# Kernel tuning notes

Measured on AMD Instinct MI355X. Metric: run time of the kernel, lower is better.

The kernel has to match this reference:

```python
import jax, jax.numpy as jnp
import numpy as np

DECAY = 0.8
EPS = 1e-05


def setup_inputs() -> dict:
    key = jax.random.key(0)
    k_x, k_e = jax.random.split(key)
    x = jax.random.normal(k_x, (8, 4096, 256), dtype=jnp.float32)
    embed = jax.random.normal(k_e, (8192, 256), dtype=jnp.float32)
    cluster_size = jnp.zeros((8192,), dtype=jnp.float32)
    embed_avg = embed  # buffer initialized as embed.clone()
    return {"x": x, "embed": embed, "cluster_size": cluster_size, "embed_avg": embed_avg}


def reference(x, embed, cluster_size, embed_avg):
    shape = x.shape
    K, d = embed.shape
    flatten = x.reshape(-1, d)  # [N, d]

    dist = -(jnp.sum(flatten * flatten, axis=1, keepdims=True)
             - 2.0 * (flatten @ embed.T)
             + jnp.sum(embed * embed, axis=1)[None, :])  # [N, K]
    embed_ind = jnp.argmax(dist, axis=-1)  # [N]

    quantize = jnp.take(embed, embed_ind, axis=0).reshape(shape)
    embed_ind_out = embed_ind.reshape(shape[:-1])

    # Training-mode EMA update (one_hot sum / one_hot matmul expressed as scatter-adds)
    counts = jnp.zeros((K,), dtype=x.dtype).at[embed_ind].add(1.0)  # embed_onehot.sum(0)
    embed_sum = jnp.zeros((K, d), dtype=x.dtype).at[embed_ind].add(flatten)  # (flatten^T @ onehot)^T

    new_cluster_size = cluster_size * DECAY + counts * (1.0 - DECAY)
    new_embed_avg = embed_avg * DECAY + embed_sum * (1.0 - DECAY)

    smoothed = (new_cluster_size + EPS) / (new_cluster_size.sum() + K * EPS) * new_cluster_size.sum()
    new_embed = new_embed_avg / smoothed[:, None]

    return quantize, embed_ind_out, new_cluster_size, new_embed_avg, new_embed
```

## Files before the change

### kernel.cpp

```cpp
#include <hip/hip_runtime.h>

#define N_ROWS 32768
#define DIM    256
#define KCODES 8192
#define DECAYF 0.8f
#define OMDF   0.2f
#define EPSF   1e-5f

#define Q_OFF    0
#define IND_OFF  8388608
#define CS_OFF   8421376
#define EA_OFF   8429568
#define NE_OFF   10526720


#define WS_E2    0
#define WS_CNT   8192
#define WS_START 16384
#define WS_CUR   24576
#define WS_SUM   40960

typedef _Float16 half8 __attribute__((ext_vector_type(8)));
typedef float floatx16 __attribute__((ext_vector_type(16)));

#define GLOAD16(g, l) __builtin_amdgcn_global_load_lds( \
    (const __attribute__((address_space(1))) void*)(g), \
    (__attribute__((address_space(3))) void*)(l), 16, 0, 0)

__global__ void zero1_kernel(const float* __restrict__ cs,
                             float* __restrict__ out, float* __restrict__ ws) {
  __shared__ float red[4];
  const int t = threadIdx.x;
  int g = blockIdx.x * blockDim.x + t;
  unsigned long long* gbest = (unsigned long long*)(out + EA_OFF);
  gbest[g] = 0ULL;
  if (g < KCODES) ((int*)(ws + WS_CNT))[g] = 0;
  if (blockIdx.x == 0) {
    float s = 0.0f;
    for (int j = t; j < KCODES; j += 256) s += cs[j];
    #pragma unroll
    for (int o = 32; o; o >>= 1) s += __shfl_xor(s, o);
    if ((t & 63) == 0) red[t >> 6] = s;
    __syncthreads();
    if (t == 0) ws[WS_SUM] = red[0] + red[1] + red[2] + red[3];
  }
}

#define PREP_ROWS 32
__global__ void prep_x_kernel(const float* __restrict__ x,
                              _Float16* __restrict__ Xp) {
  __shared__ __align__(16) _Float16 L[PREP_ROWS][264];
  const int t = threadIdx.x;
  const int row0 = blockIdx.x * PREP_ROWS;
  #pragma unroll
  for (int it = 0; it < 8; ++it) {
    int idx = it * 256 + t;
    int r = idx >> 6, q = idx & 63;
    float4 v = *(const float4*)&x[(size_t)(row0 + r) * DIM + q * 4];
    L[r][q * 4 + 0] = (_Float16)v.x;
    L[r][q * 4 + 1] = (_Float16)v.y;
    L[r][q * 4 + 2] = (_Float16)v.z;
    L[r][q * 4 + 3] = (_Float16)v.w;
  }
  __syncthreads();
  #pragma unroll
  for (int it = 0; it < 4; ++it) {
    int idx = it * 256 + t;
    int slot = idx >> 5, r = idx & 31;
    *(float4*)&Xp[((size_t)slot * N_ROWS + row0 + r) * 8] =
        *(const float4*)&L[r][slot * 8];
  }
}

__global__ void prep_e_kernel(const float* __restrict__ embed,
                              _Float16* __restrict__ Ep,
                              float* __restrict__ e2) {
  __shared__ __align__(16) _Float16 L[PREP_ROWS][264];
  const int t = threadIdx.x;
  const int row0 = blockIdx.x * PREP_ROWS;
  #pragma unroll
  for (int it = 0; it < 8; ++it) {
    int idx = it * 256 + t;
    int r = idx >> 6, q = idx & 63;
    float4 v = *(const float4*)&embed[(size_t)(row0 + r) * DIM + q * 4];
    L[r][q * 4 + 0] = (_Float16)v.x;
    L[r][q * 4 + 1] = (_Float16)v.y;
    L[r][q * 4 + 2] = (_Float16)v.z;
    L[r][q * 4 + 3] = (_Float16)v.w;
    float ssq = v.x * v.x + v.y * v.y + v.z * v.z + v.w * v.w;
    #pragma unroll
    for (int o = 32; o; o >>= 1) ssq += __shfl_xor(ssq, o);
    if ((t & 63) == 0) e2[row0 + r] = ssq;
  }
  __syncthreads();
  #pragma unroll
  for (int it = 0; it < 4; ++it) {
    int idx = it * 256 + t;
    int slot = idx >> 5, r = idx & 31;
    *(float4*)&Ep[((size_t)slot * KCODES + row0 + r) * 8] =
        *(const float4*)&L[r][slot * 8];
  }
}

__global__ __launch_bounds__(512, 2) void main_kernel(
    const _Float16* __restrict__ Xp, const _Float16* __restrict__ Ep,
    const float* __restrict__ e2, unsigned long long* __restrict__ gbest) {
  __shared__ __align__(16) _Float16 As[4 * 4 * 256 * 8];
  __shared__ __align__(16) _Float16 Bs[4 * 4 * 256 * 8];
  __shared__ __align__(16) float e2s[256];

  const int t = threadIdx.x;
  const int w = t >> 6;
  const int lane = t & 63;
  const int l31 = lane & 31;
  const int h = lane >> 5;
  const int wm = w >> 2;
  const int wn = w & 3;

  const int bid = blockIdx.x;
  const int bi = bid >> 3;
  const int cb = (bid & 7) * 4 + (bi >> 5);
  const int rbg = bi & 31;
  const int codes0 = cb * 256;
  const int rowbase = rbg * 1024;

  const bool isA = (w < 4);
  const int slot = isA ? w : (w - 4);

  auto stage = [&](int s) {
    const int buf = s & 3;
    const int se = (s & 7) * 4 + slot;
    if (isA) {
      const _Float16* src = Ep + ((size_t)se * KCODES + codes0 + lane) * 8;
      _Float16* dst = &As[buf * 8192 + slot * 2048];
      #pragma unroll
      for (int q = 0; q < 4; ++q)
        GLOAD16(src + q * 512, dst + q * 512);
    } else {
      const int row0 = rowbase + (s >> 3) * 256;
      const _Float16* src = Xp + ((size_t)se * N_ROWS + row0 + lane) * 8;
      _Float16* dst = &Bs[buf * 8192 + slot * 2048];
      #pragma unroll
      for (int q = 0; q < 4; ++q)
        GLOAD16(src + q * 512, dst + q * 512);
    }
  };

  if (t < 64) {
    float4 v = *(const float4*)&e2[codes0 + t * 4];
    *(float4*)&e2s[t * 4] = v;
  }
  __builtin_amdgcn_sched_barrier(0);
  stage(0);
  stage(1);
  asm volatile("s_waitcnt vmcnt(4)" ::: "memory");
  asm volatile("s_waitcnt lgkmcnt(0)" ::: "memory");
  __builtin_amdgcn_s_barrier();
  __builtin_amdgcn_sched_barrier(0);

  floatx16 acc[4][2];
  unsigned long long pbest[4][2];

  #pragma unroll
  for (int tile = 0; tile < 4; ++tile) {
    #pragma unroll
    for (int ct = 0; ct < 4; ++ct) {
      const int cl = wm * 128 + ct * 32 + 4 * h;
      #pragma unroll
      for (int rq = 0; rq < 4; ++rq) {
        float4 v = *(const float4*)&e2s[cl + rq * 8];
        acc[ct][0][rq * 4 + 0] = -0.5f * v.x;
        acc[ct][0][rq * 4 + 1] = -0.5f * v.y;
        acc[ct][0][rq * 4 + 2] = -0.5f * v.z;
        acc[ct][0][rq * 4 + 3] = -0.5f * v.w;
      }
      acc[ct][1] = acc[ct][0];
    }

    #pragma unroll 1
    for (int i = 0; i < 8; ++i) {
      const int s = tile * 8 + i;
      if (s + 2 < 32) stage(s + 2);
      __builtin_amdgcn_sched_barrier(0);

      const int cur = (i & 3) * 8192;
      #pragma unroll
      for (int ks = 0; ks < 2; ++ks) {
        const int sbase = cur + (2 * ks + h) * 2048;
        half8 a0 = *(const half8*)&As[sbase + (wm * 128 + l31) * 8];
        half8 a1 = *(const half8*)&As[sbase + (wm * 128 + 32 + l31) * 8];
        half8 a2 = *(const half8*)&As[sbase + (wm * 128 + 64 + l31) * 8];
        half8 a3 = *(const half8*)&As[sbase + (wm * 128 + 96 + l31) * 8];
        half8 b0 = *(const half8*)&Bs[sbase + (wn * 64 + l31) * 8];
        half8 b1 = *(const half8*)&Bs[sbase + (wn * 64 + 32 + l31) * 8];
        __builtin_amdgcn_s_setprio(1);
        acc[0][0] = __builtin_amdgcn_mfma_f32_32x32x16_f16(a0, b0, acc[0][0], 0, 0, 0);
        acc[0][1] = __builtin_amdgcn_mfma_f32_32x32x16_f16(a0, b1, acc[0][1], 0, 0, 0);
        acc[1][0] = __builtin_amdgcn_mfma_f32_32x32x16_f16(a1, b0, acc[1][0], 0, 0, 0);
        acc[1][1] = __builtin_amdgcn_mfma_f32_32x32x16_f16(a1, b1, acc[1][1], 0, 0, 0);
        acc[2][0] = __builtin_amdgcn_mfma_f32_32x32x16_f16(a2, b0, acc[2][0], 0, 0, 0);
        acc[2][1] = __builtin_amdgcn_mfma_f32_32x32x16_f16(a2, b1, acc[2][1], 0, 0, 0);
        acc[3][0] = __builtin_amdgcn_mfma_f32_32x32x16_f16(a3, b0, acc[3][0], 0, 0, 0);
        acc[3][1] = __builtin_amdgcn_mfma_f32_32x32x16_f16(a3, b1, acc[3][1], 0, 0, 0);
        __builtin_amdgcn_s_setprio(0);
      }
      __builtin_amdgcn_sched_barrier(0);

      if (s < 31) {
        if (s < 30) {
          asm volatile("s_waitcnt vmcnt(4)" ::: "memory");
        } else {
          asm volatile("s_waitcnt vmcnt(0)" ::: "memory");
        }
        __builtin_amdgcn_s_barrier();
        __builtin_amdgcn_sched_barrier(0);
      }
    }

    #pragma unroll
    for (int rt = 0; rt < 2; ++rt) {
      float best = -3.0e38f;
      int bidx = 0;
      #pragma unroll
      for (int ct = 0; ct < 4; ++ct) {
        const int cbase = codes0 + wm * 128 + ct * 32 + 4 * h;
        #pragma unroll
        for (int r = 0; r < 16; ++r) {
          const int code = cbase + (r & 3) + 8 * (r >> 2);
          float v = acc[ct][rt][r];
          if (v > best || (v == best && code < bidx)) { best = v; bidx = code; }
        }
      }
      unsigned u = __float_as_uint(best);
      u = (u & 0x80000000u) ? ~u : (u | 0x80000000u);
      unsigned long long p =
          ((unsigned long long)u << 32) | (unsigned)(8191 - bidx);
      unsigned long long op = (unsigned long long)__shfl_xor((long long)p, 32);
      if (op > p) p = op;
      pbest[tile][rt] = p;
    }
  }

  #pragma unroll
  for (int tile = 0; tile < 4; ++tile)
    #pragma unroll
    for (int rt = 0; rt < 2; ++rt)
      if (h == 0)
        atomicMax(&gbest[rowbase + tile * 256 + wn * 64 + rt * 32 + l31],
                  pbest[tile][rt]);
}

__global__ void finish_q_kernel(const float* __restrict__ embed,
                                const unsigned long long* __restrict__ gbest,
                                float* __restrict__ out, int* __restrict__ cnt) {
  const int lane = threadIdx.x & 63;
  const int wave = (blockIdx.x * blockDim.x + threadIdx.x) >> 6;
  for (int row = wave; row < N_ROWS; row += 2048) {
    unsigned long long p = gbest[row];
    int k = 8191 - (int)(unsigned)(p & 0xFFFFFFFFull);
    float4 ev = *(const float4*)&embed[(size_t)k * DIM + lane * 4];
    *(float4*)&out[Q_OFF + (size_t)row * DIM + lane * 4] = ev;
    if (lane == 0) {
      out[IND_OFF + row] = (float)k;
      atomicAdd(&cnt[k], 1);
    }
  }
}

__global__ void prefix_kernel(const int* __restrict__ cnt,
                              int* __restrict__ start,
                              int* __restrict__ cursor) {
  __shared__ int part[1024];
  const int t = threadIdx.x;
  int loc[8];
  int s = 0;
  #pragma unroll
  for (int j = 0; j < 8; ++j) { loc[j] = cnt[t * 8 + j]; s += loc[j]; }
  part[t] = s;
  __syncthreads();
  for (int off = 1; off < 1024; off <<= 1) {
    int v = (t >= off) ? part[t - off] : 0;
    __syncthreads();
    part[t] += v;
    __syncthreads();
  }
  int base = part[t] - s;
  #pragma unroll
  for (int j = 0; j < 8; ++j) {
    start[t * 8 + j] = base;
    cursor[t * 8 + j] = base;
    base += loc[j];
  }
}

__global__ void scatter_rows_kernel(const float* __restrict__ out,
                                    int* __restrict__ cursor,
                                    int* __restrict__ rowlist) {
  int r = blockIdx.x * blockDim.x + threadIdx.x;
  int k = (int)out[IND_OFF + r];
  int pos = atomicAdd(&cursor[k], 1);
  rowlist[pos] = r;
}

__global__ void bucket_sum_kernel(const float* __restrict__ x,
                                  const float* __restrict__ cs,
                                  const int* __restrict__ start,
                                  const int* __restrict__ cnt,
                                  const int* __restrict__ rowlist,
                                  float* __restrict__ out) {
  const int lane = threadIdx.x & 63;
  const int k = blockIdx.x * 4 + (threadIdx.x >> 6);
  const int s = start[k];
  const int n = cnt[k];
  float4 acc = make_float4(0.f, 0.f, 0.f, 0.f);
  int i = 0;
  for (; i + 2 <= n; i += 2) {
    int r0 = rowlist[s + i];
    int r1 = rowlist[s + i + 1];
    float4 v0 = *(const float4*)&x[(size_t)r0 * DIM + lane * 4];
    float4 v1 = *(const float4*)&x[(size_t)r1 * DIM + lane * 4];
    acc.x += v0.x + v1.x; acc.y += v0.y + v1.y;
    acc.z += v0.z + v1.z; acc.w += v0.w + v1.w;
  }
  if (i < n) {
    int r0 = rowlist[s + i];
    float4 v0 = *(const float4*)&x[(size_t)r0 * DIM + lane * 4];
    acc.x += v0.x; acc.y += v0.y; acc.z += v0.z; acc.w += v0.w;
  }
  *(float4*)&out[NE_OFF + (size_t)k * DIM + lane * 4] = acc;
  if (lane == 0) out[CS_OFF + k] = cs[k] * DECAYF + (float)n * OMDF;
}

__global__ void final2_kernel(const float* __restrict__ embed_avg,
                              float* __restrict__ out,
                              const float* __restrict__ ws_sum) {
  const float S = DECAYF * (*ws_sum) + OMDF * (float)N_ROWS;
  const float scale = S / (S + (float)KCODES * EPSF);
  int it = blockIdx.x * blockDim.x + threadIdx.x;
  int k = it >> 6;
  float ncs = out[CS_OFF + k];
  float4 ea = *(const float4*)&embed_avg[(size_t)it * 4];
  float4 es = *(const float4*)&out[NE_OFF + (size_t)it * 4];
  float4 nea;
  nea.x = ea.x * DECAYF + es.x * OMDF;
  nea.y = ea.y * DECAYF + es.y * OMDF;
  nea.z = ea.z * DECAYF + es.z * OMDF;
  nea.w = ea.w * DECAYF + es.w * OMDF;
  *(float4*)&out[EA_OFF + (size_t)it * 4] = nea;
  float inv_sm = 1.0f / ((ncs + EPSF) * scale);
  float4 ne;
  ne.x = nea.x * inv_sm;
  ne.y = nea.y * inv_sm;
  ne.z = nea.z * inv_sm;
  ne.w = nea.w * inv_sm;
  *(float4*)&out[NE_OFF + (size_t)it * 4] = ne;
}

extern "C" void kernel_launch(void* const* d_in, const int* in_sizes, int n_in,
                              void* d_out, int out_size, void* d_ws, size_t ws_size,
                              hipStream_t stream) {
  const float* x = (const float*)d_in[0];
  const float* embed = (const float*)d_in[1];
  const float* cs = (const float*)d_in[2];
  const float* ea = (const float*)d_in[3];
  float* out = (float*)d_out;
  float* ws = (float*)d_ws;

  float* e2 = ws + WS_E2;
  int* cnt = (int*)(ws + WS_CNT);
  int* start = (int*)(ws + WS_START);
  int* cursor = (int*)(ws + WS_CUR);
  float* ws_sum = ws + WS_SUM;

  _Float16* Xp = (_Float16*)(out + Q_OFF);
  unsigned long long* gbest = (unsigned long long*)(out + EA_OFF);
  int* rowlist = (int*)(out + EA_OFF);
  _Float16* Ep = (_Float16*)(out + EA_OFF + 65536);

  zero1_kernel<<<128, 256, 0, stream>>>(cs, out, ws);
  prep_x_kernel<<<N_ROWS / PREP_ROWS, 256, 0, stream>>>(x, Xp);
  prep_e_kernel<<<KCODES / PREP_ROWS, 256, 0, stream>>>(embed, Ep, e2);
  main_kernel<<<1024, 512, 0, stream>>>(Xp, Ep, e2, gbest);
  finish_q_kernel<<<512, 256, 0, stream>>>(embed, gbest, out, cnt);
  prefix_kernel<<<1, 1024, 0, stream>>>(cnt, start, cursor);
  scatter_rows_kernel<<<128, 256, 0, stream>>>(out, cursor, rowlist);
  bucket_sum_kernel<<<2048, 256, 0, stream>>>(x, cs, start, cnt, rowlist, out);
  final2_kernel<<<2048, 256, 0, stream>>>(ea, out, ws_sum);
}
```

Before: 389.2 us.

## Fuse prep kernels, merge bucket sum with EMA finalize, defer quantize gather

Merges the zeroing, x-prep and embed-prep kernels into one launch. Splits the old finish kernel into a light decode/count kernel and a quantize gather that now runs last. Fuses bucket summation with the EMA/normalize step so the per-code sums never round-trip through global memory. The rowlist moves into the second half of the quantize output region, since that region is only overwritten at the end, which lets the gather be deferred. This cuts launch count and an intermediate write/read, at the cost of a more intricate schedule for reusing the output buffer.

```diff
diff --git a/kernel.cpp b/kernel.cpp
--- a/kernel.cpp
+++ b/kernel.cpp
@@ -27,78 +27,79 @@
     (const __attribute__((address_space(1))) void*)(g), \
     (__attribute__((address_space(3))) void*)(l), 16, 0, 0)
 
-__global__ void zero1_kernel(const float* __restrict__ cs,
-                             float* __restrict__ out, float* __restrict__ ws) {
+#define PREP_ROWS 32
+__global__ void prep_all_kernel(const float* __restrict__ x,
+                                const float* __restrict__ embed,
+                                const float* __restrict__ cs,
+                                _Float16* __restrict__ Xp,
+                                _Float16* __restrict__ Ep,
+                                float* __restrict__ out,
+                                float* __restrict__ ws) {
+  __shared__ __align__(16) _Float16 L[PREP_ROWS][264];
   __shared__ float red[4];
   const int t = threadIdx.x;
-  int g = blockIdx.x * blockDim.x + t;
-  unsigned long long* gbest = (unsigned long long*)(out + EA_OFF);
-  gbest[g] = 0ULL;
-  if (g < KCODES) ((int*)(ws + WS_CNT))[g] = 0;
-  if (blockIdx.x == 0) {
-    float s = 0.0f;
-    for (int j = t; j < KCODES; j += 256) s += cs[j];
-    #pragma unroll
-    for (int o = 32; o; o >>= 1) s += __shfl_xor(s, o);
-    if ((t & 63) == 0) red[t >> 6] = s;
+  const int bid = blockIdx.x;
+
+  if (bid < 1024) {
+    if (bid < 128) {
+      unsigned long long* gbest = (unsigned long long*)(out + EA_OFF);
+      gbest[bid * 256 + t] = 0ULL;
+    } else if (bid < 160) {
+      ((int*)(ws + WS_CNT))[(bid - 128) * 256 + t] = 0;
+    }
+    const int row0 = bid * PREP_ROWS;
+    #pragma unroll
+    for (int it = 0; it < 8; ++it) {
+      int idx = it * 256 + t;
+      int r = idx >> 6, q = idx & 63;
+      float4 v = *(const float4*)&x[(size_t)(row0 + r) * DIM + q * 4];
+      L[r][q * 4 + 0] = (_Float16)v.x;
+      L[r][q * 4 + 1] = (_Float16)v.y;
+      L[r][q * 4 + 2] = (_Float16)v.z;
+      L[r][q * 4 + 3] = (_Float16)v.w;
+    }
     __syncthreads();
-    if (t == 0) ws[WS_SUM] = red[0] + red[1] + red[2] + red[3];
-  }
-}
-
-#define PREP_ROWS 32
-__global__ void prep_x_kernel(const float* __restrict__ x,
-                              _Float16* __restrict__ Xp) {
-  __shared__ __align__(16) _Float16 L[PREP_ROWS][264];
-  const int t = threadIdx.x;
-  const int row0 = blockIdx.x * PREP_ROWS;
-  #pragma unroll
-  for (int it = 0; it < 8; ++it) {
-    int idx = it * 256 + t;
-    int r = idx >> 6, q = idx & 63;
-    float4 v = *(const float4*)&x[(size_t)(row0 + r) * DIM + q * 4];
-    L[r][q * 4 + 0] = (_Float16)v.x;
-    L[r][q * 4 + 1] = (_Float16)v.y;
-    L[r][q * 4 + 2] = (_Float16)v.z;
-    L[r][q * 4 + 3] = (_Float16)v.w;
-  }
-  __syncthreads();
-  #pragma unroll
-  for (int it = 0; it < 4; ++it) {
-    int idx = it * 256 + t;
-    int slot = idx >> 5, r = idx & 31;
-    *(float4*)&Xp[((size_t)slot * N_ROWS + row0 + r) * 8] =
-        *(const float4*)&L[r][slot * 8];
-  }
-}
-
-__global__ void prep_e_kernel(const float* __restrict__ embed,
-                              _Float16* __restrict__ Ep,
-                              float* __restrict__ e2) {
-  __shared__ __align__(16) _Float16 L[PREP_ROWS][264];
-  const int t = threadIdx.x;
-  const int row0 = blockIdx.x * PREP_ROWS;
-  #pragma unroll
-  for (int it = 0; it < 8; ++it) {
-    int idx = it * 256 + t;
-    int r = idx >> 6, q = idx & 63;
-    float4 v = *(const float4*)&embed[(size_t)(row0 + r) * DIM + q * 4];
-    L[r][q * 4 + 0] = (_Float16)v.x;
-    L[r][q * 4 + 1] = (_Float16)v.y;
-    L[r][q * 4 + 2] = (_Float16)v.z;
-    L[r][q * 4 + 3] = (_Float16)v.w;
-    float ssq = v.x * v.x + v.y * v.y + v.z * v.z + v.w * v.w;
-    #pragma unroll
-    for (int o = 32; o; o >>= 1) ssq += __shfl_xor(ssq, o);
-    if ((t & 63) == 0) e2[row0 + r] = ssq;
-  }
-  __syncthreads();
-  #pragma unroll
-  for (int it = 0; it < 4; ++it) {
-    int idx = it * 256 + t;
-    int slot = idx >> 5, r = idx & 31;
-    *(float4*)&Ep[((size_t)slot * KCODES + row0 + r) * 8] =
-        *(const float4*)&L[r][slot * 8];
+    #pragma unroll
+    for (int it = 0; it < 4; ++it) {
+      int idx = it * 256 + t;
+      int slot = idx >> 5, r = idx & 31;
+      *(float4*)&Xp[((size_t)slot * N_ROWS + row0 + r) * 8] =
+          *(const float4*)&L[r][slot * 8];
+    }
+  } else {
+    const int row0 = (bid - 1024) * PREP_ROWS;
+    float* e2 = ws + WS_E2;
+    #pragma unroll
+    for (int it = 0; it < 8; ++it) {
+      int idx = it * 256 + t;
+      int r = idx >> 6, q = idx & 63;
+      float4 v = *(const float4*)&embed[(size_t)(row0 + r) * DIM + q * 4];
+      L[r][q * 4 + 0] = (_Float16)v.x;
+      L[r][q * 4 + 1] = (_Float16)v.y;
+      L[r][q * 4 + 2] = (_Float16)v.z;
+      L[r][q * 4 + 3] = (_Float16)v.w;
+      float ssq = v.x * v.x + v.y * v.y + v.z * v.z + v.w * v.w;
+      #pragma unroll
+      for (int o = 32; o; o >>= 1) ssq += __shfl_xor(ssq, o);
+      if ((t & 63) == 0) e2[row0 + r] = ssq;
+    }
+    if (bid == 1024) {
+      float s = 0.0f;
+      for (int j = t; j < KCODES; j += 256) s += cs[j];
+      #pragma unroll
+      for (int o = 32; o; o >>= 1) s += __shfl_xor(s, o);
+      if ((t & 63) == 0) red[t >> 6] = s;
+    }
+    __syncthreads();
+    if (bid == 1024 && t == 0)
+      ws[WS_SUM] = red[0] + red[1] + red[2] + red[3];
+    #pragma unroll
+    for (int it = 0; it < 4; ++it) {
+      int idx = it * 256 + t;
+      int slot = idx >> 5, r = idx & 31;
+      *(float4*)&Ep[((size_t)slot * KCODES + row0 + r) * 8] =
+          *(const float4*)&L[r][slot * 8];
+    }
   }
 }
 
@@ -250,21 +251,14 @@
                   pbest[tile][rt]);
 }
 
-__global__ void finish_q_kernel(const float* __restrict__ embed,
-                                const unsigned long long* __restrict__ gbest,
-                                float* __restrict__ out, int* __restrict__ cnt) {
-  const int lane = threadIdx.x & 63;
-  const int wave = (blockIdx.x * blockDim.x + threadIdx.x) >> 6;
-  for (int row = wave; row < N_ROWS; row += 2048) {
-    unsigned long long p = gbest[row];
-    int k = 8191 - (int)(unsigned)(p & 0xFFFFFFFFull);
-    float4 ev = *(const float4*)&embed[(size_t)k * DIM + lane * 4];
-    *(float4*)&out[Q_OFF + (size_t)row * DIM + lane * 4] = ev;
-    if (lane == 0) {
-      out[IND_OFF + row] = (float)k;
-      atomicAdd(&cnt[k], 1);
-    }
-  }
+__global__ void decode_count_kernel(const unsigned long long* __restrict__ gbest,
+                                    float* __restrict__ out,
+                                    int* __restrict__ cnt) {
+  int r = blockIdx.x * blockDim.x + threadIdx.x;
+  unsigned long long p = gbest[r];
+  int k = 8191 - (int)(unsigned)(p & 0xFFFFFFFFull);
+  out[IND_OFF + r] = (float)k;
+  atomicAdd(&cnt[k], 1);
 }
 
 __global__ void prefix_kernel(const int* __restrict__ cnt,
@@ -302,12 +296,14 @@
   rowlist[pos] = r;
 }
 
-__global__ void bucket_sum_kernel(const float* __restrict__ x,
-                                  const float* __restrict__ cs,
-                                  const int* __restrict__ start,
-                                  const int* __restrict__ cnt,
-                                  const int* __restrict__ rowlist,
-                                  float* __restrict__ out) {
+__global__ void bucket_final_kernel(const float* __restrict__ x,
+                                    const float* __restrict__ cs,
+                                    const float* __restrict__ embed_avg,
+                                    const int* __restrict__ start,
+                                    const int* __restrict__ cnt,
+                                    const int* __restrict__ rowlist,
+                                    float* __restrict__ out,
+                                    const float* __restrict__ ws_sum) {
   const int lane = threadIdx.x & 63;
   const int k = blockIdx.x * 4 + (threadIdx.x >> 6);
   const int s = start[k];
@@ -327,33 +323,35 @@
     float4 v0 = *(const float4*)&x[(size_t)r0 * DIM + lane * 4];
     acc.x += v0.x; acc.y += v0.y; acc.z += v0.z; acc.w += v0.w;
   }
-  *(float4*)&out[NE_OFF + (size_t)k * DIM + lane * 4] = acc;
-  if (lane == 0) out[CS_OFF + k] = cs[k] * DECAYF + (float)n * OMDF;
-}
-
-__global__ void final2_kernel(const float* __restrict__ embed_avg,
-                              float* __restrict__ out,
-                              const float* __restrict__ ws_sum) {
   const float S = DECAYF * (*ws_sum) + OMDF * (float)N_ROWS;
   const float scale = S / (S + (float)KCODES * EPSF);
-  int it = blockIdx.x * blockDim.x + threadIdx.x;
-  int k = it >> 6;
-  float ncs = out[CS_OFF + k];
-  float4 ea = *(const float4*)&embed_avg[(size_t)it * 4];
-  float4 es = *(const float4*)&out[NE_OFF + (size_t)it * 4];
+  float ncs = cs[k] * DECAYF + (float)n * OMDF;
+  if (lane == 0) out[CS_OFF + k] = ncs;
+  float4 ea = *(const float4*)&embed_avg[(size_t)k * DIM + lane * 4];
   float4 nea;
-  nea.x = ea.x * DECAYF + es.x * OMDF;
-  nea.y = ea.y * DECAYF + es.y * OMDF;
-  nea.z = ea.z * DECAYF + es.z * OMDF;
-  nea.w = ea.w * DECAYF + es.w * OMDF;
-  *(float4*)&out[EA_OFF + (size_t)it * 4] = nea;
+  nea.x = ea.x * DECAYF + acc.x * OMDF;
+  nea.y = ea.y * DECAYF + acc.y * OMDF;
+  nea.z = ea.z * DECAYF + acc.z * OMDF;
+  nea.w = ea.w * DECAYF + acc.w * OMDF;
+  *(float4*)&out[EA_OFF + (size_t)k * DIM + lane * 4] = nea;
   float inv_sm = 1.0f / ((ncs + EPSF) * scale);
   float4 ne;
   ne.x = nea.x * inv_sm;
   ne.y = nea.y * inv_sm;
   ne.z = nea.z * inv_sm;
   ne.w = nea.w * inv_sm;
-  *(float4*)&out[NE_OFF + (size_t)it * 4] = ne;
+  *(float4*)&out[NE_OFF + (size_t)k * DIM + lane * 4] = ne;
+}
+
+__global__ void finish_q_kernel(const float* __restrict__ embed,
+                                float* __restrict__ out) {
+  const int lane = threadIdx.x & 63;
+  const int wave = (blockIdx.x * blockDim.x + threadIdx.x) >> 6;
+  for (int row = wave; row < N_ROWS; row += 2048) {
+    int k = (int)out[IND_OFF + row];
+    float4 ev = *(const float4*)&embed[(size_t)k * DIM + lane * 4];
+    *(float4*)&out[Q_OFF + (size_t)row * DIM + lane * 4] = ev;
+  }
 }
 
 extern "C" void kernel_launch(void* const* d_in, const int* in_sizes, int n_in,
@@ -373,17 +371,16 @@
   float* ws_sum = ws + WS_SUM;
 
   _Float16* Xp = (_Float16*)(out + Q_OFF);
+  int* rowlist = (int*)(out + Q_OFF + 4194304);
   unsigned long long* gbest = (unsigned long long*)(out + EA_OFF);
-  int* rowlist = (int*)(out + EA_OFF);
   _Float16* Ep = (_Float16*)(out + EA_OFF + 65536);
 
-  zero1_kernel<<<128, 256, 0, stream>>>(cs, out, ws);
-  prep_x_kernel<<<N_ROWS / PREP_ROWS, 256, 0, stream>>>(x, Xp);
-  prep_e_kernel<<<KCODES / PREP_ROWS, 256, 0, stream>>>(embed, Ep, e2);
+  prep_all_kernel<<<1280, 256, 0, stream>>>(x, embed, cs, Xp, Ep, out, ws);
   main_kernel<<<1024, 512, 0, stream>>>(Xp, Ep, e2, gbest);
-  finish_q_kernel<<<512, 256, 0, stream>>>(embed, gbest, out, cnt);
+  decode_count_kernel<<<128, 256, 0, stream>>>(gbest, out, cnt);
   prefix_kernel<<<1, 1024, 0, stream>>>(cnt, start, cursor);
   scatter_rows_kernel<<<128, 256, 0, stream>>>(out, cursor, rowlist);
-  bucket_sum_kernel<<<2048, 256, 0, stream>>>(x, cs, start, cnt, rowlist, out);
-  final2_kernel<<<2048, 256, 0, stream>>>(ea, out, ws_sum);
-}
+  bucket_final_kernel<<<2048, 256, 0, stream>>>(x, cs, ea, start, cnt,
+                                                rowlist, out, ws_sum);
+  finish_q_kernel<<<512, 256, 0, stream>>>(embed, out);
+}
```

Result: no change. 384.5 us (-1.2%).
